# Kernel optimization log

Measured on AMD Instinct MI355X. Metric: run time of the kernel, lower is better.

## Reference

```python
import jax, jax.numpy as jnp
import numpy as np

N, F, C, E = 1024, 64, 4, 32768
H = 256       # MLP hidden width
C_OUT = 4     # new edge channels produced by nn_edge


def setup_inputs() -> dict:
    key = jax.random.key(0)
    ks = jax.random.split(key, 12)
    x = jax.random.normal(ks[0], (N, F), dtype=jnp.float32)
    edge_index = jax.random.randint(ks[1], (C, 2, E), 0, N)
    edge_weight = jax.random.uniform(ks[2], (C, E), dtype=jnp.float32)
    s_n1 = 1.0 / np.sqrt(C * F)
    s_n2 = 1.0 / np.sqrt(H)
    s_e1 = 1.0 / np.sqrt(C + 2 * F)
    return {
        "x": x,
        "edge_index": edge_index,
        "edge_weight": edge_weight,
        "Wn1": jax.random.normal(ks[3], (C * F, H), dtype=jnp.float32) * s_n1,
        "bn1": jnp.zeros((H,), jnp.float32),
        "Wn2": jax.random.normal(ks[4], (H, F), dtype=jnp.float32) * s_n2,
        "bn2": jnp.zeros((F,), jnp.float32),
        "We1": jax.random.normal(ks[5], (C + 2 * F, H), dtype=jnp.float32) * s_e1,
        "be1": jnp.zeros((H,), jnp.float32),
        "We2": jax.random.normal(ks[6], (H, C_OUT), dtype=jnp.float32) * s_n2,
        "be2": jnp.zeros((C_OUT,), jnp.float32),
        "eps": jnp.zeros((), jnp.float32),
    }


def reference(x, edge_index, edge_weight, Wn1, bn1, Wn2, bn2, We1, be1, We2, be2, eps):
    # ---- MCGNN: per-channel edge-weighted scatter-add aggregation ----
    def agg_one(ei, w):
        # ei: [2,E] (row0 = source j, row1 = target i); w: [E]
        msg = x[ei[0]] * w[:, None]                       # [E,F]
        return jax.ops.segment_sum(msg, ei[1], num_segments=N)  # [N,F]

    agg = jax.vmap(agg_one)(edge_index, edge_weight)      # [C,N,F]
    out_cat = agg + (1.0 + eps) * x                       # broadcast self term
    h = out_cat.transpose(1, 0, 2).reshape(N, C * F)      # [N, C*F]
    x_next = jax.nn.relu(h @ Wn1 + bn1) @ Wn2 + bn2       # [N,F]

    # ---- EDPGNN: dense adjacency per channel + broadcast x_i/x_j ----
    def dense_adj(ei, w):
        return jnp.zeros((N, N), x.dtype).at[ei[0], ei[1]].add(w)

    a = jax.vmap(dense_adj)(edge_index, edge_weight)      # [C,N,N]
    a = a.transpose(1, 2, 0)                              # [N,N,C]
    x_i = jnp.broadcast_to(x_next[:, None, :], (N, N, F))
    x_j = jnp.broadcast_to(x_next[None, :, :], (N, N, F))
    feat = jnp.concatenate([a, x_i, x_j], axis=2).reshape(N * N, C + 2 * F)
    adj_out = (jax.nn.relu(feat @ We1 + be1) @ We2 + be2).reshape(N, N, C_OUT)
    return adj_out
```

## Files before the change

### kernel.cpp

```cpp
#include <hip/hip_runtime.h>

#define NN 1024
#define FF 64
#define CC 4
#define EE 32768
#define HH 256

#define OFF_ADENSE 0u
#define OFF_CNT    4194304u
#define OFF_OFFS   4198400u
#define OFF_CURSOR 4202512u
#define OFF_SRTS   4206608u
#define OFF_SRTW   4337680u
#define OFF_AGG    4468752u
#define OFF_HID    4194304u
#define OFF_XN     4730896u
#define OFF_P      4796432u
#define OFF_Q      5058576u

__global__ __launch_bounds__(256)
void k_count(const int* __restrict__ ei, int* __restrict__ cnt)
{
    unsigned t = blockIdx.x * 256u + threadIdx.x;
    unsigned e = t & (EE - 1u);
    unsigned c = t >> 15;
    int dst = ei[c * 2 * EE + EE + e];
    atomicAdd(&cnt[c * NN + dst], 1);
}

__global__ __launch_bounds__(1024)
void k_scan(const int* __restrict__ cnt, int* __restrict__ offs, int* __restrict__ cursor)
{
    __shared__ int sums[1024];
    const int t = threadIdx.x;
    int c0 = cnt[t * 4], c1 = cnt[t * 4 + 1], c2 = cnt[t * 4 + 2], c3 = cnt[t * 4 + 3];
    int s = c0 + c1 + c2 + c3;
    sums[t] = s;
    __syncthreads();
    for (int d = 1; d < 1024; d <<= 1) {
        int v = (t >= d) ? sums[t - d] : 0;
        __syncthreads();
        sums[t] += v;
        __syncthreads();
    }
    int base = sums[t] - s;
    offs[t * 4]     = base;           cursor[t * 4]     = base;
    offs[t * 4 + 1] = base + c0;      cursor[t * 4 + 1] = base + c0;
    offs[t * 4 + 2] = base + c0 + c1; cursor[t * 4 + 2] = base + c0 + c1;
    offs[t * 4 + 3] = base + c0 + c1 + c2; cursor[t * 4 + 3] = base + c0 + c1 + c2;
    if (t == 1023) offs[4096] = sums[1023];
}

__global__ __launch_bounds__(256)
void k_bucket(const int* __restrict__ ei, const float* __restrict__ ew,
              int* __restrict__ cursor, int* __restrict__ srt_src, float* __restrict__ srt_w)
{
    unsigned t = blockIdx.x * 256u + threadIdx.x;
    unsigned e = t & (EE - 1u);
    unsigned c = t >> 15;
    int src = ei[c * 2 * EE + e];
    int dst = ei[c * 2 * EE + EE + e];
    float w = ew[c * EE + e];
    int pos = atomicAdd(&cursor[c * NN + dst], 1);
    srt_src[pos] = src;
    srt_w[pos] = w;
}

__global__ __launch_bounds__(256)
void k_agg_gather(const float* __restrict__ x, const int* __restrict__ offs,
                  const int* __restrict__ srt_src, const float* __restrict__ srt_w,
                  float* __restrict__ agg)
{
    const int g = blockIdx.x * 4 + (threadIdx.x >> 6);
    const int lane = threadIdx.x & 63;
    const int c = g >> 10, dst = g & 1023;
    const int beg = offs[g], end = offs[g + 1];
    float acc = 0.f;
    for (int k = beg; k < end; ++k) {
        int src = srt_src[k];
        float w = srt_w[k];
        acc += x[src * FF + lane] * w;
    }
    agg[dst * (CC * FF) + c * FF + lane] = acc;
}

__global__ __launch_bounds__(256)
void k_adj_scatter(const int* __restrict__ ei, const float* __restrict__ ew,
                   float* __restrict__ adense)
{
    unsigned t = blockIdx.x * 256u + threadIdx.x;
    unsigned e = t & (EE - 1u);
    unsigned c = t >> 15;
    int i = ei[c * 2 * EE + e];
    int j = ei[c * 2 * EE + EE + e];
    float w = ew[c * EE + e];
    atomicAdd(&adense[(i * NN + j) * CC + c], w);
}

__global__ __launch_bounds__(1024)
void k_node_mlp1(const float* __restrict__ agg, const float* __restrict__ x,
                 const float* __restrict__ Wn1, const float* __restrict__ bn1,
                 const float* __restrict__ epsp, float* __restrict__ hid)
{
    __shared__ float hval[4][256];
    const int tid = threadIdx.x;
    const int nn = tid >> 8, h = tid & 255;
    const int n0 = blockIdx.x * 4;
    const float ope = 1.0f + epsp[0];
    hval[nn][h] = agg[(n0 + nn) * 256 + h] + ope * x[(n0 + nn) * 64 + (h & 63)];
    __syncthreads();
    float acc = bn1[h];
#pragma unroll 8
    for (int k = 0; k < 256; ++k)
        acc += hval[nn][k] * Wn1[k * 256 + h];
    hid[(n0 + nn) * 256 + h] = fmaxf(acc, 0.f);
}

__global__ __launch_bounds__(512)
void k_node_mlp2(const float* __restrict__ hid, const float* __restrict__ Wn2,
                 const float* __restrict__ bn2, float* __restrict__ xn)
{
    __shared__ float hl[8][256];
    const int tid = threadIdx.x;
    const int n0 = blockIdx.x * 8;
    for (int u = tid; u < 2048; u += 512) hl[u >> 8][u & 255] = hid[n0 * 256 + u];
    __syncthreads();
    const int nn = tid >> 6, f = tid & 63;
    float acc = bn2[f];
#pragma unroll 8
    for (int k = 0; k < 256; ++k)
        acc += hl[nn][k] * Wn2[k * 64 + f];
    xn[(n0 + nn) * 64 + f] = acc;
}

__global__ __launch_bounds__(1024)
void k_pq(const float* __restrict__ xn, const float* __restrict__ We1,
          const float* __restrict__ be1, float* __restrict__ P, float* __restrict__ Q)
{
    __shared__ float xl[4][64];
    const int tid = threadIdx.x;
    const int r = tid >> 8, h = tid & 255;
    const int n0 = blockIdx.x * 4;
    if (tid < 256) xl[tid >> 6][tid & 63] = xn[n0 * 64 + tid];
    __syncthreads();
    float p = be1[h], q = 0.f;
#pragma unroll 8
    for (int f = 0; f < 64; ++f) {
        float xv = xl[r][f];
        p += xv * We1[(4 + f) * 256 + h];
        q += xv * We1[(68 + f) * 256 + h];
    }
    P[(n0 + r) * 256 + h] = p;
    Q[(n0 + r) * 256 + h] = q;
}

__global__ __launch_bounds__(256, 4)
void k_edge_mlp(const float* __restrict__ P, const float* __restrict__ Q,
                const float* __restrict__ adense, const float* __restrict__ We1,
                const float* __restrict__ We2, const float* __restrict__ be2,
                float* __restrict__ out)
{
    __shared__ float4 Pl[32 * 16];
    __shared__ float4 Ql[32 * 16];
    __shared__ float4 W1l[4 * 16];
    __shared__ float4 W2l[64];

    const int tid = threadIdx.x;
    const int tx = tid & 15, ty = tid >> 4;
    const int iBase = blockIdx.y * 32, jBase = blockIdx.x * 32;
    const int psw = ty & 7;
    const int qsw = tx & 7;

    float4 a[2][2], acc[2][2];
#pragma unroll
    for (int ii = 0; ii < 2; ++ii)
#pragma unroll
        for (int jj = 0; jj < 2; ++jj) {
            a[ii][jj] = *(const float4*)(adense +
                ((size_t)(iBase + ty * 2 + ii) * NN + (jBase + tx * 2 + jj)) * 4);
            acc[ii][jj] = make_float4(0.f, 0.f, 0.f, 0.f);
        }

    for (int hc = 0; hc < 4; ++hc) {
        __syncthreads();
#pragma unroll
        for (int u = 0; u < 2; ++u) {
            int idx = tid + u * 256;
            int row = idx >> 4, q = idx & 15;
            int ph = q ^ ((row >> 1) & 7);
            Pl[row * 16 + ph] = *(const float4*)(P + (iBase + row) * 256 + hc * 64 + q * 4);
            Ql[row * 16 + ph] = *(const float4*)(Q + (jBase + row) * 256 + hc * 64 + q * 4);
        }
        if (tid < 64) {
            int c = tid >> 4, q = tid & 15;
            W1l[tid] = *(const float4*)(We1 + c * 256 + hc * 64 + q * 4);
        } else if (tid < 128) {
            int h = tid - 64;
            W2l[h] = *(const float4*)(We2 + (hc * 64 + h) * 4);
        }
        __syncthreads();

        for (int q = 0; q < 16; ++q) {
            float4 p[2], qv[2], w1[4], w2[4];
#pragma unroll
            for (int r = 0; r < 2; ++r) p[r]  = Pl[(ty * 2 + r) * 16 + (q ^ psw)];
#pragma unroll
            for (int r = 0; r < 2; ++r) qv[r] = Ql[(tx * 2 + r) * 16 + (q ^ qsw)];
#pragma unroll
            for (int c = 0; c < 4; ++c) w1[c] = W1l[c * 16 + q];
#pragma unroll
            for (int k = 0; k < 4; ++k) w2[k] = W2l[q * 4 + k];

#pragma unroll
            for (int ii = 0; ii < 2; ++ii) {
#pragma unroll
                for (int jj = 0; jj < 2; ++jj) {
                    const float4 av = a[ii][jj];
                    float s0 = av.x * w1[0].x + av.y * w1[1].x + av.z * w1[2].x + av.w * w1[3].x;
                    float s1 = av.x * w1[0].y + av.y * w1[1].y + av.z * w1[2].y + av.w * w1[3].y;
                    float s2 = av.x * w1[0].z + av.y * w1[1].z + av.z * w1[2].z + av.w * w1[3].z;
                    float s3 = av.x * w1[0].w + av.y * w1[1].w + av.z * w1[2].w + av.w * w1[3].w;
                    float v0 = fmaxf(p[ii].x + qv[jj].x + s0, 0.f);
                    float v1 = fmaxf(p[ii].y + qv[jj].y + s1, 0.f);
                    float v2 = fmaxf(p[ii].z + qv[jj].z + s2, 0.f);
                    float v3 = fmaxf(p[ii].w + qv[jj].w + s3, 0.f);
                    acc[ii][jj].x += v0 * w2[0].x + v1 * w2[1].x + v2 * w2[2].x + v3 * w2[3].x;
                    acc[ii][jj].y += v0 * w2[0].y + v1 * w2[1].y + v2 * w2[2].y + v3 * w2[3].y;
                    acc[ii][jj].z += v0 * w2[0].z + v1 * w2[1].z + v2 * w2[2].z + v3 * w2[3].z;
                    acc[ii][jj].w += v0 * w2[0].w + v1 * w2[1].w + v2 * w2[2].w + v3 * w2[3].w;
                }
            }
        }
    }

    const float4 b2 = *(const float4*)be2;
#pragma unroll
    for (int ii = 0; ii < 2; ++ii)
#pragma unroll
        for (int jj = 0; jj < 2; ++jj) {
            float4 o = acc[ii][jj];
            o.x += b2.x; o.y += b2.y; o.z += b2.z; o.w += b2.w;
            *(float4*)(out + ((size_t)(iBase + ty * 2 + ii) * NN + (jBase + tx * 2 + jj)) * 4) = o;
        }
}

extern "C" void kernel_launch(void* const* d_in, const int* in_sizes, int n_in,
                              void* d_out, int out_size, void* d_ws, size_t ws_size,
                              hipStream_t stream)
{
    (void)in_sizes; (void)n_in; (void)out_size; (void)ws_size;
    const float* x   = (const float*)d_in[0];
    const int*   ei  = (const int*)d_in[1];
    const float* ew  = (const float*)d_in[2];
    const float* Wn1 = (const float*)d_in[3];
    const float* bn1 = (const float*)d_in[4];
    const float* Wn2 = (const float*)d_in[5];
    const float* bn2 = (const float*)d_in[6];
    const float* We1 = (const float*)d_in[7];
    const float* be1 = (const float*)d_in[8];
    const float* We2 = (const float*)d_in[9];
    const float* be2 = (const float*)d_in[10];
    const float* eps = (const float*)d_in[11];
    float* out = (float*)d_out;

    float* ws = (float*)d_ws;
    float* adense = ws + OFF_ADENSE;
    int*   cnt    = (int*)(ws + OFF_CNT);
    int*   offs   = (int*)(ws + OFF_OFFS);
    int*   cursor = (int*)(ws + OFF_CURSOR);
    int*   srts   = (int*)(ws + OFF_SRTS);
    float* srtw   = ws + OFF_SRTW;
    float* agg    = ws + OFF_AGG;
    float* hid    = ws + OFF_HID;
    float* xn     = ws + OFF_XN;
    float* Pb     = ws + OFF_P;
    float* Qb     = ws + OFF_Q;

    hipMemsetAsync(d_ws, 0, (size_t)(4194304 + 4096) * sizeof(float), stream);

    k_count      <<<(CC * EE) / 256, 256, 0, stream>>>(ei, cnt);
    k_scan       <<<1, 1024, 0, stream>>>(cnt, offs, cursor);
    k_bucket     <<<(CC * EE) / 256, 256, 0, stream>>>(ei, ew, cursor, srts, srtw);
    k_adj_scatter<<<(CC * EE) / 256, 256, 0, stream>>>(ei, ew, adense);
    k_agg_gather <<<(CC * NN) / 4, 256, 0, stream>>>(x, offs, srts, srtw, agg);
    k_node_mlp1  <<<NN / 4, 1024, 0, stream>>>(agg, x, Wn1, bn1, eps, hid);
    k_node_mlp2  <<<NN / 8, 512, 0, stream>>>(hid, Wn2, bn2, xn);
    k_pq         <<<NN / 4, 1024, 0, stream>>>(xn, We1, be1, Pb, Qb);

    dim3 g(NN / 32, NN / 32);
    k_edge_mlp<<<g, 256, 0, stream>>>(Pb, Qb, adense, We1, We2, be2, out);
}
```

Before: 257.5 us.

## Fuse node pipeline into one kernel, merge bucket with adjacency scatter, warp-shuffle scan

Merges the edge bucketing and dense-adjacency atomic scatter into one pass over the edges. The gather aggregation, both node MLP layers and the P/Q projection now run in a single kernel that keeps intermediates in shared memory, so agg, hid and xn are no longer written to and reread from global memory. The prefix scan changes from a 1024-thread shared-memory Hillis-Steele loop to 256 threads using wave shuffles. The edge MLP now reads We1/We2 from global memory (expected to hit in cache) instead of staging them in LDS. The intent is to cut launch count and global round-trips, at the cost of less parallelism in the fused node kernel and weight loads inside the edge MLP's inner loop.

```diff
diff --git a/kernel.cpp b/kernel.cpp
--- a/kernel.cpp
+++ b/kernel.cpp
@@ -12,11 +12,8 @@
 #define OFF_CURSOR 4202512u
 #define OFF_SRTS   4206608u
 #define OFF_SRTW   4337680u
-#define OFF_AGG    4468752u
-#define OFF_HID    4194304u
-#define OFF_XN     4730896u
-#define OFF_P      4796432u
-#define OFF_Q      5058576u
+#define OFF_P      4468752u
+#define OFF_Q      4730896u
 
 __global__ __launch_bounds__(256)
 void k_count(const int* __restrict__ ei, int* __restrict__ cnt)
@@ -28,32 +25,45 @@
     atomicAdd(&cnt[c * NN + dst], 1);
 }
 
-__global__ __launch_bounds__(1024)
+__global__ __launch_bounds__(256)
 void k_scan(const int* __restrict__ cnt, int* __restrict__ offs, int* __restrict__ cursor)
 {
-    __shared__ int sums[1024];
+    __shared__ int wsum[4];
     const int t = threadIdx.x;
-    int c0 = cnt[t * 4], c1 = cnt[t * 4 + 1], c2 = cnt[t * 4 + 2], c3 = cnt[t * 4 + 3];
-    int s = c0 + c1 + c2 + c3;
-    sums[t] = s;
-    __syncthreads();
-    for (int d = 1; d < 1024; d <<= 1) {
-        int v = (t >= d) ? sums[t - d] : 0;
-        __syncthreads();
-        sums[t] += v;
-        __syncthreads();
-    }
-    int base = sums[t] - s;
-    offs[t * 4]     = base;           cursor[t * 4]     = base;
-    offs[t * 4 + 1] = base + c0;      cursor[t * 4 + 1] = base + c0;
-    offs[t * 4 + 2] = base + c0 + c1; cursor[t * 4 + 2] = base + c0 + c1;
-    offs[t * 4 + 3] = base + c0 + c1 + c2; cursor[t * 4 + 3] = base + c0 + c1 + c2;
-    if (t == 1023) offs[4096] = sums[1023];
+    int c[16];
+    int s = 0;
+    const int4* cp = (const int4*)(cnt + t * 16);
+#pragma unroll
+    for (int u = 0; u < 4; ++u) {
+        int4 v = cp[u];
+        c[u * 4 + 0] = v.x; c[u * 4 + 1] = v.y; c[u * 4 + 2] = v.z; c[u * 4 + 3] = v.w;
+        s += v.x + v.y + v.z + v.w;
+    }
+    int incl = s;
+#pragma unroll
+    for (int d = 1; d < 64; d <<= 1) {
+        int v = __shfl_up(incl, d, 64);
+        if ((t & 63) >= d) incl += v;
+    }
+    const int w = t >> 6;
+    if ((t & 63) == 63) wsum[w] = incl;
+    __syncthreads();
+    int base = incl - s;
+    for (int ww = 0; ww < w; ++ww) base += wsum[ww];
+    int run = base;
+#pragma unroll
+    for (int u = 0; u < 16; ++u) {
+        offs[t * 16 + u] = run;
+        cursor[t * 16 + u] = run;
+        run += c[u];
+    }
+    if (t == 255) offs[4096] = run;
 }
 
 __global__ __launch_bounds__(256)
-void k_bucket(const int* __restrict__ ei, const float* __restrict__ ew,
-              int* __restrict__ cursor, int* __restrict__ srt_src, float* __restrict__ srt_w)
+void k_bucket_adj(const int* __restrict__ ei, const float* __restrict__ ew,
+                  int* __restrict__ cursor, int* __restrict__ srt_src,
+                  float* __restrict__ srt_w, float* __restrict__ adense)
 {
     unsigned t = blockIdx.x * 256u + threadIdx.x;
     unsigned e = t & (EE - 1u);
@@ -64,94 +74,76 @@
     int pos = atomicAdd(&cursor[c * NN + dst], 1);
     srt_src[pos] = src;
     srt_w[pos] = w;
-}
-
-__global__ __launch_bounds__(256)
-void k_agg_gather(const float* __restrict__ x, const int* __restrict__ offs,
-                  const int* __restrict__ srt_src, const float* __restrict__ srt_w,
-                  float* __restrict__ agg)
-{
-    const int g = blockIdx.x * 4 + (threadIdx.x >> 6);
-    const int lane = threadIdx.x & 63;
-    const int c = g >> 10, dst = g & 1023;
-    const int beg = offs[g], end = offs[g + 1];
-    float acc = 0.f;
-    for (int k = beg; k < end; ++k) {
-        int src = srt_src[k];
-        float w = srt_w[k];
-        acc += x[src * FF + lane] * w;
-    }
-    agg[dst * (CC * FF) + c * FF + lane] = acc;
-}
-
-__global__ __launch_bounds__(256)
-void k_adj_scatter(const int* __restrict__ ei, const float* __restrict__ ew,
-                   float* __restrict__ adense)
-{
-    unsigned t = blockIdx.x * 256u + threadIdx.x;
-    unsigned e = t & (EE - 1u);
-    unsigned c = t >> 15;
-    int i = ei[c * 2 * EE + e];
-    int j = ei[c * 2 * EE + EE + e];
-    float w = ew[c * EE + e];
-    atomicAdd(&adense[(i * NN + j) * CC + c], w);
+    atomicAdd(&adense[((size_t)src * NN + dst) * CC + c], w);
 }
 
 __global__ __launch_bounds__(1024)
-void k_node_mlp1(const float* __restrict__ agg, const float* __restrict__ x,
-                 const float* __restrict__ Wn1, const float* __restrict__ bn1,
-                 const float* __restrict__ epsp, float* __restrict__ hid)
+void k_node(const float* __restrict__ x, const int* __restrict__ offs,
+            const int* __restrict__ srt_src, const float* __restrict__ srt_w,
+            const float* __restrict__ Wn1, const float* __restrict__ bn1,
+            const float* __restrict__ Wn2, const float* __restrict__ bn2,
+            const float* __restrict__ We1, const float* __restrict__ be1,
+            const float* __restrict__ epsp,
+            float* __restrict__ P, float* __restrict__ Q)
 {
     __shared__ float hval[4][256];
+    __shared__ float hidl[4][256];
+    __shared__ float part[4][4][64];
+    __shared__ float xnl[4][64];
     const int tid = threadIdx.x;
-    const int nn = tid >> 8, h = tid & 255;
     const int n0 = blockIdx.x * 4;
-    const float ope = 1.0f + epsp[0];
-    hval[nn][h] = agg[(n0 + nn) * 256 + h] + ope * x[(n0 + nn) * 64 + (h & 63)];
-    __syncthreads();
-    float acc = bn1[h];
+
+    {
+        const int w = tid >> 6, lane = tid & 63;
+        const int c = w & 3, nn = w >> 2;
+        const int g = c * NN + (n0 + nn);
+        const int beg = offs[g], end = offs[g + 1];
+        float acc = 0.f;
+        for (int k = beg; k < end; ++k)
+            acc += x[srt_src[k] * FF + lane] * srt_w[k];
+        const float ope = 1.0f + epsp[0];
+        hval[nn][c * 64 + lane] = acc + ope * x[(n0 + nn) * FF + lane];
+    }
+    __syncthreads();
+
+    {
+        const int nn = tid >> 8, h = tid & 255;
+        float acc = bn1[h];
 #pragma unroll 8
-    for (int k = 0; k < 256; ++k)
-        acc += hval[nn][k] * Wn1[k * 256 + h];
-    hid[(n0 + nn) * 256 + h] = fmaxf(acc, 0.f);
-}
-
-__global__ __launch_bounds__(512)
-void k_node_mlp2(const float* __restrict__ hid, const float* __restrict__ Wn2,
-                 const float* __restrict__ bn2, float* __restrict__ xn)
-{
-    __shared__ float hl[8][256];
-    const int tid = threadIdx.x;
-    const int n0 = blockIdx.x * 8;
-    for (int u = tid; u < 2048; u += 512) hl[u >> 8][u & 255] = hid[n0 * 256 + u];
-    __syncthreads();
-    const int nn = tid >> 6, f = tid & 63;
-    float acc = bn2[f];
+        for (int k = 0; k < 256; ++k)
+            acc += hval[nn][k] * Wn1[k * 256 + h];
+        hidl[nn][h] = fmaxf(acc, 0.f);
+    }
+    __syncthreads();
+
+    {
+        const int kq = tid >> 8, nn = (tid >> 6) & 3, f = tid & 63;
+        float p = 0.f;
 #pragma unroll 8
-    for (int k = 0; k < 256; ++k)
-        acc += hl[nn][k] * Wn2[k * 64 + f];
-    xn[(n0 + nn) * 64 + f] = acc;
-}
-
-__global__ __launch_bounds__(1024)
-void k_pq(const float* __restrict__ xn, const float* __restrict__ We1,
-          const float* __restrict__ be1, float* __restrict__ P, float* __restrict__ Q)
-{
-    __shared__ float xl[4][64];
-    const int tid = threadIdx.x;
-    const int r = tid >> 8, h = tid & 255;
-    const int n0 = blockIdx.x * 4;
-    if (tid < 256) xl[tid >> 6][tid & 63] = xn[n0 * 64 + tid];
-    __syncthreads();
-    float p = be1[h], q = 0.f;
+        for (int k = kq * 64; k < kq * 64 + 64; ++k)
+            p += hidl[nn][k] * Wn2[k * 64 + f];
+        part[kq][nn][f] = p;
+    }
+    __syncthreads();
+    if (tid < 256) {
+        const int nn = tid >> 6, f = tid & 63;
+        xnl[nn][f] = bn2[f] + part[0][nn][f] + part[1][nn][f]
+                             + part[2][nn][f] + part[3][nn][f];
+    }
+    __syncthreads();
+
+    {
+        const int r = tid >> 8, h = tid & 255;
+        float p = be1[h], q = 0.f;
 #pragma unroll 8
-    for (int f = 0; f < 64; ++f) {
-        float xv = xl[r][f];
-        p += xv * We1[(4 + f) * 256 + h];
-        q += xv * We1[(68 + f) * 256 + h];
-    }
-    P[(n0 + r) * 256 + h] = p;
-    Q[(n0 + r) * 256 + h] = q;
+        for (int f = 0; f < 64; ++f) {
+            float xv = xnl[r][f];
+            p += xv * We1[(4 + f) * 256 + h];
+            q += xv * We1[(68 + f) * 256 + h];
+        }
+        P[(n0 + r) * 256 + h] = p;
+        Q[(n0 + r) * 256 + h] = q;
+    }
 }
 
 __global__ __launch_bounds__(256, 4)
@@ -162,8 +154,6 @@
 {
     __shared__ float4 Pl[32 * 16];
     __shared__ float4 Ql[32 * 16];
-    __shared__ float4 W1l[4 * 16];
-    __shared__ float4 W2l[64];
 
     const int tid = threadIdx.x;
     const int tx = tid & 15, ty = tid >> 4;
@@ -191,25 +181,22 @@
             Pl[row * 16 + ph] = *(const float4*)(P + (iBase + row) * 256 + hc * 64 + q * 4);
             Ql[row * 16 + ph] = *(const float4*)(Q + (jBase + row) * 256 + hc * 64 + q * 4);
         }
-        if (tid < 64) {
-            int c = tid >> 4, q = tid & 15;
-            W1l[tid] = *(const float4*)(We1 + c * 256 + hc * 64 + q * 4);
-        } else if (tid < 128) {
-            int h = tid - 64;
-            W2l[h] = *(const float4*)(We2 + (hc * 64 + h) * 4);
-        }
         __syncthreads();
 
         for (int q = 0; q < 16; ++q) {
-            float4 p[2], qv[2], w1[4], w2[4];
+            float4 w1[4], w2[4];
+#pragma unroll
+            for (int c = 0; c < 4; ++c)
+                w1[c] = *(const float4*)(We1 + c * 256 + hc * 64 + q * 4);
+#pragma unroll
+            for (int k = 0; k < 4; ++k)
+                w2[k] = *(const float4*)(We2 + (hc * 64 + q * 4 + k) * 4);
+
+            float4 p[2], qv[2];
 #pragma unroll
             for (int r = 0; r < 2; ++r) p[r]  = Pl[(ty * 2 + r) * 16 + (q ^ psw)];
 #pragma unroll
             for (int r = 0; r < 2; ++r) qv[r] = Ql[(tx * 2 + r) * 16 + (q ^ qsw)];
-#pragma unroll
-            for (int c = 0; c < 4; ++c) w1[c] = W1l[c * 16 + q];
-#pragma unroll
-            for (int k = 0; k < 4; ++k) w2[k] = W2l[q * 4 + k];
 
 #pragma unroll
             for (int ii = 0; ii < 2; ++ii) {
@@ -270,22 +257,16 @@
     int*   cursor = (int*)(ws + OFF_CURSOR);
     int*   srts   = (int*)(ws + OFF_SRTS);
     float* srtw   = ws + OFF_SRTW;
-    float* agg    = ws + OFF_AGG;
-    float* hid    = ws + OFF_HID;
-    float* xn     = ws + OFF_XN;
     float* Pb     = ws + OFF_P;
     float* Qb     = ws + OFF_Q;
 
     hipMemsetAsync(d_ws, 0, (size_t)(4194304 + 4096) * sizeof(float), stream);
 
-    k_count      <<<(CC * EE) / 256, 256, 0, stream>>>(ei, cnt);
-    k_scan       <<<1, 1024, 0, stream>>>(cnt, offs, cursor);
-    k_bucket     <<<(CC * EE) / 256, 256, 0, stream>>>(ei, ew, cursor, srts, srtw);
-    k_adj_scatter<<<(CC * EE) / 256, 256, 0, stream>>>(ei, ew, adense);
-    k_agg_gather <<<(CC * NN) / 4, 256, 0, stream>>>(x, offs, srts, srtw, agg);
-    k_node_mlp1  <<<NN / 4, 1024, 0, stream>>>(agg, x, Wn1, bn1, eps, hid);
-    k_node_mlp2  <<<NN / 8, 512, 0, stream>>>(hid, Wn2, bn2, xn);
-    k_pq         <<<NN / 4, 1024, 0, stream>>>(xn, We1, be1, Pb, Qb);
+    k_count     <<<(CC * EE) / 256, 256, 0, stream>>>(ei, cnt);
+    k_scan      <<<1, 256, 0, stream>>>(cnt, offs, cursor);
+    k_bucket_adj<<<(CC * EE) / 256, 256, 0, stream>>>(ei, ew, cursor, srts, srtw, adense);
+    k_node      <<<NN / 4, 1024, 0, stream>>>(x, offs, srts, srtw,
+                                              Wn1, bn1, Wn2, bn2, We1, be1, eps, Pb, Qb);
 
     dim3 g(NN / 32, NN / 32);
     k_edge_mlp<<<g, 256, 0, stream>>>(Pb, Qb, adense, We1, We2, be2, out);
```

New measurement: 237.3 us. 7.8% less time.
